# Kernel optimization log

Hardware: AMD Instinct MI355X
Metric: run time of the kernel (lower is better)

The kernel has to match this reference:

```python
import jax, jax.numpy as jnp
import numpy as np

BATCH = 4096
DIM = 128
TEMP = 0.5
EPS = 1e-12  # F.normalize eps


def setup_inputs() -> dict:
    key = jax.random.key(0)
    k1, k2 = jax.random.split(key)
    emb_i = jax.random.normal(k1, (BATCH, DIM), dtype=jnp.float32)
    emb_j = jax.random.normal(k2, (BATCH, DIM), dtype=jnp.float32)
    return {"emb_i": emb_i, "emb_j": emb_j}


def _l2_normalize(x):
    # matches torch.nn.functional.normalize(x, dim=1, eps=1e-12)
    n = jnp.maximum(jnp.linalg.norm(x, axis=1, keepdims=True), EPS)
    return x / n


def reference(emb_i, emb_j):
    B = BATCH
    z_i = _l2_normalize(emb_i)
    z_j = _l2_normalize(emb_j)
    reps = jnp.concatenate([z_i, z_j], axis=0)            # [2B, D]
    # cosine similarity of unit vectors == Gram matrix
    sim = reps @ reps.T                                   # [2B, 2B]
    sim_ij = jnp.diagonal(sim, offset=B)                  # [B]
    sim_ji = jnp.diagonal(sim, offset=-B)                 # [B]
    positives = jnp.concatenate([sim_ij, sim_ji], axis=0) # [2B]
    neg_mask = 1.0 - jnp.eye(2 * B, dtype=sim.dtype)
    denom = jnp.sum(neg_mask * jnp.exp(sim / TEMP), axis=1)  # [2B]
    # -log(exp(pos/T) / denom) == -pos/T + log(denom)
    loss_partial = -(positives / TEMP) + jnp.log(denom)
    loss = jnp.sum(loss_partial) / (2 * B * 5)
    return loss
```

## Files before the change

### kernel.cpp

```cpp
#include <hip/hip_runtime.h>
#include <hip/hip_bf16.h>

#define B_ROWS 4096
#define DIMN 128
#define N2 8192
#define SQRT_CEXP 1.6986436f

using f32x4 = __attribute__((ext_vector_type(4))) float;
using i32x4 = __attribute__((ext_vector_type(4))) int;
using i32x8 = __attribute__((ext_vector_type(8))) int;
typedef long i64;


__global__ __launch_bounds__(256) void normpos_k(const float* __restrict__ emb_i,
                                                 const float* __restrict__ emb_j,
                                                 i64* __restrict__ zt,
                                                 float* __restrict__ pospart,
                                                 float* __restrict__ out) {
    const int t = threadIdx.x;
    if (blockIdx.x == 0 && t == 0) out[0] = 0.f;
    const int lr = t >> 4;
    const int s  = t & 15;
    const int p  = blockIdx.x * 16 + lr;
    const float4* ai = (const float4*)(emb_i + (size_t)p * DIMN + s * 8);
    const float4* bj = (const float4*)(emb_j + (size_t)p * DIMN + s * 8);
    float4 a0 = ai[0], a1 = ai[1];
    float4 b0 = bj[0], b1 = bj[1];
    float sa = a0.x*a0.x + a0.y*a0.y + a0.z*a0.z + a0.w*a0.w
             + a1.x*a1.x + a1.y*a1.y + a1.z*a1.z + a1.w*a1.w;
    float sb = b0.x*b0.x + b0.y*b0.y + b0.z*b0.z + b0.w*b0.w
             + b1.x*b1.x + b1.y*b1.y + b1.z*b1.z + b1.w*b1.w;
    float dp = a0.x*b0.x + a0.y*b0.y + a0.z*b0.z + a0.w*b0.w
             + a1.x*b1.x + a1.y*b1.y + a1.z*b1.z + a1.w*b1.w;
    #pragma unroll
    for (int d = 1; d < 16; d <<= 1) {
        sa += __shfl_xor(sa, d);
        sb += __shfl_xor(sb, d);
        dp += __shfl_xor(dp, d);
    }
    float ia = __builtin_amdgcn_rsqf(fmaxf(sa, 1e-24f));
    float ib = __builtin_amdgcn_rsqf(fmaxf(sb, 1e-24f));
    float fa = ia * SQRT_CEXP, fb = ib * SQRT_CEXP;

    int wa0 = __builtin_amdgcn_cvt_pk_fp8_f32(a0.x * fa, a0.y * fa, 0, false);
    wa0     = __builtin_amdgcn_cvt_pk_fp8_f32(a0.z * fa, a0.w * fa, wa0, true);
    int wa1 = __builtin_amdgcn_cvt_pk_fp8_f32(a1.x * fa, a1.y * fa, 0, false);
    wa1     = __builtin_amdgcn_cvt_pk_fp8_f32(a1.z * fa, a1.w * fa, wa1, true);
    i64 qa = ((i64)(unsigned)wa1 << 32) | (unsigned)wa0;
    int wb0 = __builtin_amdgcn_cvt_pk_fp8_f32(b0.x * fb, b0.y * fb, 0, false);
    wb0     = __builtin_amdgcn_cvt_pk_fp8_f32(b0.z * fb, b0.w * fb, wb0, true);
    int wb1 = __builtin_amdgcn_cvt_pk_fp8_f32(b1.x * fb, b1.y * fb, 0, false);
    wb1     = __builtin_amdgcn_cvt_pk_fp8_f32(b1.z * fb, b1.w * fb, wb1, true);
    i64 qb = ((i64)(unsigned)wb1 << 32) | (unsigned)wb0;

    const int slot = ((s >> 2) * 16 + lr) * 4 + (s & 3);
    zt[(size_t)blockIdx.x * 256 + slot] = qa;
    zt[(size_t)(256 + blockIdx.x) * 256 + slot] = qb;

    __shared__ float red[16];
    if (s == 0) red[lr] = dp * ia * ib;
    __syncthreads();
    if (t == 0) {
        float x = 0.f;
        #pragma unroll
        for (int i = 0; i < 16; ++i) x += red[i];
        pospart[blockIdx.x] = x;
    }
}

template <bool MASK>
__device__ __forceinline__ void accum_step(const f32x4 (&acc)[2][2],
                                           float (&ps)[2][4],
                                           int rb, int cb, int rq, int fr) {
    #pragma unroll
    for (int m = 0; m < 2; ++m)
        #pragma unroll
        for (int n = 0; n < 2; ++n)
            #pragma unroll
            for (int j = 0; j < 4; ++j) {
                float e = __builtin_amdgcn_exp2f(acc[m][n][j]);
                if (MASK) {
                    if (rb + m * 16 + rq + j == cb + n * 16 + fr) e = 0.f;
                }
                ps[m][j] += e;
            }
}

__global__ __launch_bounds__(256) void gram_k(const char* __restrict__ zt,
                                              float* __restrict__ rowpart) {
    const int t = threadIdx.x;
    const int lane = t & 63;
    const int w = t >> 6;
    const int p = blockIdx.x >> 2;
    const int e = blockIdx.x & 3;
    const int rb = p * 32;
    const int fr = lane & 15;
    const int rq = (lane >> 4) * 4;

    const char* pa = zt + (size_t)(p * 2) * 2048 + lane * 32;
    const char* pb = zt + (size_t)(e * 128 + w * 32) * 2048 + lane * 32;

    i32x4 Alo[2], Ahi[2];
    #pragma unroll
    for (int m = 0; m < 2; ++m) {
        asm volatile("global_load_dwordx4 %0, %1, off"
                     : "=v"(Alo[m]) : "v"(pa + (size_t)m * 2048));
        asm volatile("global_load_dwordx4 %0, %1, off offset:16"
                     : "=v"(Ahi[m]) : "v"(pa + (size_t)m * 2048));
    }
    i32x4 Blo[2][2], Bhi[2][2];
    #pragma unroll
    for (int n = 0; n < 2; ++n) {
        asm volatile("global_load_dwordx4 %0, %1, off"
                     : "=v"(Blo[0][n]) : "v"(pb + (size_t)n * 2048));
        asm volatile("global_load_dwordx4 %0, %1, off offset:16"
                     : "=v"(Bhi[0][n]) : "v"(pb + (size_t)n * 2048));
    }
    asm volatile("s_waitcnt vmcnt(4)" ::: "memory");
    __builtin_amdgcn_sched_barrier(0);
    i32x8 A8[2];
    #pragma unroll
    for (int m = 0; m < 2; ++m)
        A8[m] = __builtin_shufflevector(Alo[m], Ahi[m], 0, 1, 2, 3, 4, 5, 6, 7);

    float ps[2][4] = {};
    #pragma unroll
    for (int s = 0; s < 16; ++s) {
        if (s < 15) {
            const char* pn = pb + (size_t)(s + 1) * 4096;
            #pragma unroll
            for (int n = 0; n < 2; ++n) {
                asm volatile("global_load_dwordx4 %0, %1, off"
                             : "=v"(Blo[(s + 1) & 1][n]) : "v"(pn + (size_t)n * 2048));
                asm volatile("global_load_dwordx4 %0, %1, off offset:16"
                             : "=v"(Bhi[(s + 1) & 1][n]) : "v"(pn + (size_t)n * 2048));
            }
            asm volatile("s_waitcnt vmcnt(4)" ::: "memory");
        } else {
            asm volatile("s_waitcnt vmcnt(0)" ::: "memory");
        }
        __builtin_amdgcn_sched_barrier(0);

        f32x4 acc[2][2] = {};
        __builtin_amdgcn_s_setprio(1);
        #pragma unroll
        for (int n = 0; n < 2; ++n) {
            i32x8 B8 = __builtin_shufflevector(Blo[s & 1][n], Bhi[s & 1][n],
                                               0, 1, 2, 3, 4, 5, 6, 7);
            #pragma unroll
            for (int m = 0; m < 2; ++m)
                acc[m][n] = __builtin_amdgcn_mfma_scale_f32_16x16x128_f8f6f4(
                    A8[m], B8, acc[m][n], 0, 0,
                    0, 0x7f7f7f7f, 0, 0x7f7f7f7f);
        }
        __builtin_amdgcn_s_setprio(0);

        const int cb = e * 2048 + w * 512 + s * 32;
        if (cb == rb) accum_step<true >(acc, ps, rb, cb, rq, fr);
        else          accum_step<false>(acc, ps, rb, cb, rq, fr);
    }

    #pragma unroll
    for (int m = 0; m < 2; ++m)
        #pragma unroll
        for (int j = 0; j < 4; ++j) {
            float v = ps[m][j];
            #pragma unroll
            for (int d = 1; d < 16; d <<= 1) v += __shfl_xor(v, d);
            ps[m][j] = v;
        }
    __shared__ float red[4][32];
    if (fr == 0) {
        #pragma unroll
        for (int m = 0; m < 2; ++m)
            #pragma unroll
            for (int j = 0; j < 4; ++j)
                red[w][m * 16 + rq + j] = ps[m][j];
    }
    __syncthreads();
    if (t < 32)
        rowpart[e * N2 + rb + t] = red[0][t] + red[1][t] + red[2][t] + red[3][t];
}

__global__ void finalize_k(const float* __restrict__ rowpart,
                           const float* __restrict__ pospart,
                           float* __restrict__ out) {
    const int t = threadIdx.x;
    const int r = blockIdx.x * 1024 + t;
    float d = rowpart[r] + rowpart[N2 + r] + rowpart[2 * N2 + r] + rowpart[3 * N2 + r];
    float acc = __builtin_amdgcn_logf(d) * 0.6931471805599453f;
    if (blockIdx.x == 0 && t < 256) acc -= 4.0f * pospart[t];
    #pragma unroll
    for (int m = 32; m; m >>= 1) acc += __shfl_xor(acc, m);
    __shared__ float red[16];
    if ((t & 63) == 0) red[t >> 6] = acc;
    __syncthreads();
    if (t == 0) {
        float x = 0.f;
        #pragma unroll
        for (int i = 0; i < 16; ++i) x += red[i];
        atomicAdd(out, x * (1.0f / (2.0f * B_ROWS * 5.0f)));
    }
}

extern "C" void kernel_launch(void* const* d_in, const int* in_sizes, int n_in,
                              void* d_out, int out_size, void* d_ws, size_t ws_size,
                              hipStream_t stream) {
    const float* emb_i = (const float*)d_in[0];
    const float* emb_j = (const float*)d_in[1];
    i64* zt        = (i64*)d_ws;
    float* rowpart = (float*)((char*)d_ws + (size_t)N2 * DIMN);
    float* pospart = rowpart + 4 * N2;

    normpos_k<<<256, 256, 0, stream>>>(emb_i, emb_j, zt, pospart, (float*)d_out);
    gram_k<<<1024, 256, 0, stream>>>((const char*)zt, rowpart);
    finalize_k<<<8, 1024, 0, stream>>>(rowpart, pospart, (float*)d_out);
}
```

Baseline: 25.83 us.

## Exploit Gram matrix symmetry to compute half the tiles with column partial sums

Adds a symmetric Gram kernel in which each block computes only half of the 32-wide diagonal tile offsets. It accumulates both row sums and column sums of exp(sim), and writes the column sums into a large colpart buffer that finalize_k sums over 127 offsets. This roughly halves the MFMA and exp work, at the cost of extra shuffles, a large workspace of about 4 MB of column partials, and a much heavier finalize pass that reads 128 strided rows per output. The old path is kept as a fallback when the workspace is too small.

```diff
diff --git a/kernel.cpp b/kernel.cpp
--- a/kernel.cpp
+++ b/kernel.cpp
@@ -70,7 +70,7 @@
 
 template <bool MASK>
 __device__ __forceinline__ void accum_step(const f32x4 (&acc)[2][2],
-                                           float (&ps)[2][4],
+                                           float (&ps)[2][4], float (&cs)[2],
                                            int rb, int cb, int rq, int fr) {
     #pragma unroll
     for (int m = 0; m < 2; ++m)
@@ -83,7 +83,153 @@
                     if (rb + m * 16 + rq + j == cb + n * 16 + fr) e = 0.f;
                 }
                 ps[m][j] += e;
+                cs[n] += e;
             }
+}
+
+__global__ __launch_bounds__(256) void gram_sym_k(const char* __restrict__ zt,
+                                                  float* __restrict__ rowpart,
+                                                  float* __restrict__ colpart) {
+    const int t = threadIdx.x;
+    const int lane = t & 63;
+    const int w = t >> 6;
+    const int p = blockIdx.x >> 2;
+    const int e = blockIdx.x & 3;
+    const int rb = p * 32;
+    const int fr = lane & 15;
+    const int rq = (lane >> 4) * 4;
+    const int dt0 = e * 32 + w * 8;
+
+    const char* pa = zt + (size_t)(p * 2) * 2048 + lane * 32;
+    auto bptr = [&](int dt) {
+        return zt + (size_t)((rb + dt * 32) & 8191) * 128 + lane * 32;
+    };
+
+    i32x4 Alo[2], Ahi[2];
+    #pragma unroll
+    for (int m = 0; m < 2; ++m) {
+        asm volatile("global_load_dwordx4 %0, %1, off"
+                     : "=v"(Alo[m]) : "v"(pa + (size_t)m * 2048));
+        asm volatile("global_load_dwordx4 %0, %1, off offset:16"
+                     : "=v"(Ahi[m]) : "v"(pa + (size_t)m * 2048));
+    }
+    i32x4 Blo[2][2], Bhi[2][2];
+    {
+        const char* p0 = bptr(dt0);
+        #pragma unroll
+        for (int n = 0; n < 2; ++n) {
+            asm volatile("global_load_dwordx4 %0, %1, off"
+                         : "=v"(Blo[0][n]) : "v"(p0 + (size_t)n * 2048));
+            asm volatile("global_load_dwordx4 %0, %1, off offset:16"
+                         : "=v"(Bhi[0][n]) : "v"(p0 + (size_t)n * 2048));
+        }
+    }
+    asm volatile("s_waitcnt vmcnt(4)" ::: "memory");
+    __builtin_amdgcn_sched_barrier(0);
+    i32x8 A8[2];
+    #pragma unroll
+    for (int m = 0; m < 2; ++m)
+        A8[m] = __builtin_shufflevector(Alo[m], Ahi[m], 0, 1, 2, 3, 4, 5, 6, 7);
+
+    float ps[2][4] = {};
+    float colsc0[8], colsc1[8];
+    #pragma unroll
+    for (int s = 0; s < 8; ++s) {
+        if (s < 7) {
+            const char* pn = bptr(dt0 + s + 1);
+            #pragma unroll
+            for (int n = 0; n < 2; ++n) {
+                asm volatile("global_load_dwordx4 %0, %1, off"
+                             : "=v"(Blo[(s + 1) & 1][n]) : "v"(pn + (size_t)n * 2048));
+                asm volatile("global_load_dwordx4 %0, %1, off offset:16"
+                             : "=v"(Bhi[(s + 1) & 1][n]) : "v"(pn + (size_t)n * 2048));
+            }
+            asm volatile("s_waitcnt vmcnt(4)" ::: "memory");
+        } else {
+            asm volatile("s_waitcnt vmcnt(0)" ::: "memory");
+        }
+        __builtin_amdgcn_sched_barrier(0);
+
+        f32x4 acc[2][2] = {};
+        __builtin_amdgcn_s_setprio(1);
+        #pragma unroll
+        for (int n = 0; n < 2; ++n) {
+            i32x8 B8 = __builtin_shufflevector(Blo[s & 1][n], Bhi[s & 1][n],
+                                               0, 1, 2, 3, 4, 5, 6, 7);
+            #pragma unroll
+            for (int m = 0; m < 2; ++m)
+                acc[m][n] = __builtin_amdgcn_mfma_scale_f32_16x16x128_f8f6f4(
+                    A8[m], B8, acc[m][n], 0, 0,
+                    0, 0x7f7f7f7f, 0, 0x7f7f7f7f);
+        }
+        __builtin_amdgcn_s_setprio(0);
+
+        const int cb = (rb + (dt0 + s) * 32) & 8191;
+        float cs[2] = {0.f, 0.f};
+        if (cb == rb) accum_step<true >(acc, ps, cs, rb, cb, rq, fr);
+        else          accum_step<false>(acc, ps, cs, rb, cb, rq, fr);
+        cs[0] += __shfl_xor(cs[0], 16); cs[0] += __shfl_xor(cs[0], 32);
+        cs[1] += __shfl_xor(cs[1], 16); cs[1] += __shfl_xor(cs[1], 32);
+        colsc0[s] = cs[0]; colsc1[s] = cs[1];
+    }
+
+    if (e == 0 && w == 0) {
+        const char* pn = bptr(128);
+        #pragma unroll
+        for (int n = 0; n < 2; ++n) {
+            asm volatile("global_load_dwordx4 %0, %1, off"
+                         : "=v"(Blo[0][n]) : "v"(pn + (size_t)n * 2048));
+            asm volatile("global_load_dwordx4 %0, %1, off offset:16"
+                         : "=v"(Bhi[0][n]) : "v"(pn + (size_t)n * 2048));
+        }
+        asm volatile("s_waitcnt vmcnt(0)" ::: "memory");
+        __builtin_amdgcn_sched_barrier(0);
+        f32x4 acc[2][2] = {};
+        #pragma unroll
+        for (int n = 0; n < 2; ++n) {
+            i32x8 B8 = __builtin_shufflevector(Blo[0][n], Bhi[0][n],
+                                               0, 1, 2, 3, 4, 5, 6, 7);
+            #pragma unroll
+            for (int m = 0; m < 2; ++m)
+                acc[m][n] = __builtin_amdgcn_mfma_scale_f32_16x16x128_f8f6f4(
+                    A8[m], B8, acc[m][n], 0, 0, 0, 0x7f7f7f7f, 0, 0x7f7f7f7f);
+        }
+        float cs[2] = {0.f, 0.f};
+        accum_step<false>(acc, ps, cs, rb, 0, rq, fr);
+    }
+
+    if (lane < 16) {
+        #pragma unroll
+        for (int s = 0; s < 8; ++s) {
+            const int dt = dt0 + s;
+            if (dt != 0) {
+                const int cbb = (rb + dt * 32) & 8191;
+                colpart[(size_t)dt * N2 + cbb + lane]      = colsc0[s];
+                colpart[(size_t)dt * N2 + cbb + 16 + lane] = colsc1[s];
+            }
+        }
+    }
+
+    #pragma unroll
+    for (int m = 0; m < 2; ++m)
+        #pragma unroll
+        for (int j = 0; j < 4; ++j) {
+            float v = ps[m][j];
+            #pragma unroll
+            for (int d = 1; d < 16; d <<= 1) v += __shfl_xor(v, d);
+            ps[m][j] = v;
+        }
+    __shared__ float red[4][32];
+    if (fr == 0) {
+        #pragma unroll
+        for (int m = 0; m < 2; ++m)
+            #pragma unroll
+            for (int j = 0; j < 4; ++j)
+                red[w][m * 16 + rq + j] = ps[m][j];
+    }
+    __syncthreads();
+    if (t < 32)
+        rowpart[e * N2 + rb + t] = red[0][t] + red[1][t] + red[2][t] + red[3][t];
 }
 
 __global__ __launch_bounds__(256) void gram_k(const char* __restrict__ zt,
@@ -150,14 +296,14 @@
             #pragma unroll
             for (int m = 0; m < 2; ++m)
                 acc[m][n] = __builtin_amdgcn_mfma_scale_f32_16x16x128_f8f6f4(
-                    A8[m], B8, acc[m][n], 0, 0,
-                    0, 0x7f7f7f7f, 0, 0x7f7f7f7f);
+                    A8[m], B8, acc[m][n], 0, 0, 0, 0x7f7f7f7f, 0, 0x7f7f7f7f);
         }
         __builtin_amdgcn_s_setprio(0);
 
         const int cb = e * 2048 + w * 512 + s * 32;
-        if (cb == rb) accum_step<true >(acc, ps, rb, cb, rq, fr);
-        else          accum_step<false>(acc, ps, rb, cb, rq, fr);
+        float cs[2] = {0.f, 0.f};
+        if (cb == rb) accum_step<true >(acc, ps, cs, rb, cb, rq, fr);
+        else          accum_step<false>(acc, ps, cs, rb, cb, rq, fr);
     }
 
     #pragma unroll
@@ -183,11 +329,13 @@
 }
 
 __global__ void finalize_k(const float* __restrict__ rowpart,
+                           const float* __restrict__ colpart,
                            const float* __restrict__ pospart,
-                           float* __restrict__ out) {
+                           float* __restrict__ out, int ncol) {
     const int t = threadIdx.x;
     const int r = blockIdx.x * 1024 + t;
     float d = rowpart[r] + rowpart[N2 + r] + rowpart[2 * N2 + r] + rowpart[3 * N2 + r];
+    for (int k = 1; k <= ncol; ++k) d += colpart[(size_t)k * N2 + r];
     float acc = __builtin_amdgcn_logf(d) * 0.6931471805599453f;
     if (blockIdx.x == 0 && t < 256) acc -= 4.0f * pospart[t];
     #pragma unroll
@@ -211,8 +359,16 @@
     i64* zt        = (i64*)d_ws;
     float* rowpart = (float*)((char*)d_ws + (size_t)N2 * DIMN);
     float* pospart = rowpart + 4 * N2;
+    float* colpart = pospart + 256;
+    const size_t need = (size_t)N2 * DIMN + (4 * N2 + 256 + 128 * N2) * sizeof(float);
+    const bool sym = ws_size >= need;
 
     normpos_k<<<256, 256, 0, stream>>>(emb_i, emb_j, zt, pospart, (float*)d_out);
-    gram_k<<<1024, 256, 0, stream>>>((const char*)zt, rowpart);
-    finalize_k<<<8, 1024, 0, stream>>>(rowpart, pospart, (float*)d_out);
-}
+    if (sym) {
+        gram_sym_k<<<1024, 256, 0, stream>>>((const char*)zt, rowpart, colpart);
+        finalize_k<<<8, 1024, 0, stream>>>(rowpart, colpart, pospart, (float*)d_out, 127);
+    } else {
+        gram_k<<<1024, 256, 0, stream>>>((const char*)zt, rowpart);
+        finalize_k<<<8, 1024, 0, stream>>>(rowpart, colpart, pospart, (float*)d_out, 0);
+    }
+}
```

Result: slower. 58.08 us (+124.9%).

## Exploit Gram matrix symmetry to halve MFMA tiles, adding column partial sums

Applied to the files above, without the earlier changes.

Each row block now computes only about half of the 32x32 tile diagonals, using a cyclic offset scheme (128 diagonals plus one extra diagonal at offset 128 handled by one wave). Each tile contributes its exp values to both row sums and column sums, since the symmetric counterpart is never computed. Column partials are written to a large colpart buffer, 128 slices of 8192 floats each. The finalize kernel now reduces all of those slices. This halves MFMA and exp work. In exchange it adds per-tile shuffles, about 4 MB of extra global writes and reads, and a heavier finalize pass.

```diff
diff --git a/kernel.cpp b/kernel.cpp
--- a/kernel.cpp
+++ b/kernel.cpp
@@ -70,7 +70,7 @@
 
 template <bool MASK>
 __device__ __forceinline__ void accum_step(const f32x4 (&acc)[2][2],
-                                           float (&ps)[2][4],
+                                           float (&ps)[2][4], float (&cs)[2],
                                            int rb, int cb, int rq, int fr) {
     #pragma unroll
     for (int m = 0; m < 2; ++m)
@@ -83,11 +83,13 @@
                     if (rb + m * 16 + rq + j == cb + n * 16 + fr) e = 0.f;
                 }
                 ps[m][j] += e;
+                cs[n] += e;
             }
 }
 
-__global__ __launch_bounds__(256) void gram_k(const char* __restrict__ zt,
-                                              float* __restrict__ rowpart) {
+__global__ __launch_bounds__(256) void gram_sym_k(const char* __restrict__ zt,
+                                                  float* __restrict__ rowpart,
+                                                  float* __restrict__ colpart) {
     const int t = threadIdx.x;
     const int lane = t & 63;
     const int w = t >> 6;
@@ -96,9 +98,12 @@
     const int rb = p * 32;
     const int fr = lane & 15;
     const int rq = (lane >> 4) * 4;
+    const int dt0 = e * 32 + w * 8;
 
     const char* pa = zt + (size_t)(p * 2) * 2048 + lane * 32;
-    const char* pb = zt + (size_t)(e * 128 + w * 32) * 2048 + lane * 32;
+    auto bptr = [&](int dt) {
+        return zt + (size_t)((rb + dt * 32) & 8191) * 128 + lane * 32;
+    };
 
     i32x4 Alo[2], Ahi[2];
     #pragma unroll
@@ -109,12 +114,15 @@
                      : "=v"(Ahi[m]) : "v"(pa + (size_t)m * 2048));
     }
     i32x4 Blo[2][2], Bhi[2][2];
-    #pragma unroll
-    for (int n = 0; n < 2; ++n) {
-        asm volatile("global_load_dwordx4 %0, %1, off"
-                     : "=v"(Blo[0][n]) : "v"(pb + (size_t)n * 2048));
-        asm volatile("global_load_dwordx4 %0, %1, off offset:16"
-                     : "=v"(Bhi[0][n]) : "v"(pb + (size_t)n * 2048));
+    {
+        const char* p0 = bptr(dt0);
+        #pragma unroll
+        for (int n = 0; n < 2; ++n) {
+            asm volatile("global_load_dwordx4 %0, %1, off"
+                         : "=v"(Blo[0][n]) : "v"(p0 + (size_t)n * 2048));
+            asm volatile("global_load_dwordx4 %0, %1, off offset:16"
+                         : "=v"(Bhi[0][n]) : "v"(p0 + (size_t)n * 2048));
+        }
     }
     asm volatile("s_waitcnt vmcnt(4)" ::: "memory");
     __builtin_amdgcn_sched_barrier(0);
@@ -124,10 +132,11 @@
         A8[m] = __builtin_shufflevector(Alo[m], Ahi[m], 0, 1, 2, 3, 4, 5, 6, 7);
 
     float ps[2][4] = {};
-    #pragma unroll
-    for (int s = 0; s < 16; ++s) {
-        if (s < 15) {
-            const char* pn = pb + (size_t)(s + 1) * 4096;
+    float colsc0[8], colsc1[8];
+    #pragma unroll
+    for (int s = 0; s < 8; ++s) {
+        if (s < 7) {
+            const char* pn = bptr(dt0 + s + 1);
             #pragma unroll
             for (int n = 0; n < 2; ++n) {
                 asm volatile("global_load_dwordx4 %0, %1, off"
@@ -155,9 +164,50 @@
         }
         __builtin_amdgcn_s_setprio(0);
 
-        const int cb = e * 2048 + w * 512 + s * 32;
-        if (cb == rb) accum_step<true >(acc, ps, rb, cb, rq, fr);
-        else          accum_step<false>(acc, ps, rb, cb, rq, fr);
+        const int cb = (rb + (dt0 + s) * 32) & 8191;
+        float cs[2] = {0.f, 0.f};
+        if (cb == rb) accum_step<true >(acc, ps, cs, rb, cb, rq, fr);
+        else          accum_step<false>(acc, ps, cs, rb, cb, rq, fr);
+        cs[0] += __shfl_xor(cs[0], 16); cs[0] += __shfl_xor(cs[0], 32);
+        cs[1] += __shfl_xor(cs[1], 16); cs[1] += __shfl_xor(cs[1], 32);
+        colsc0[s] = cs[0]; colsc1[s] = cs[1];
+    }
+
+    if (e == 0 && w == 0) {
+        const char* pn = bptr(128);
+        #pragma unroll
+        for (int n = 0; n < 2; ++n) {
+            asm volatile("global_load_dwordx4 %0, %1, off"
+                         : "=v"(Blo[0][n]) : "v"(pn + (size_t)n * 2048));
+            asm volatile("global_load_dwordx4 %0, %1, off offset:16"
+                         : "=v"(Bhi[0][n]) : "v"(pn + (size_t)n * 2048));
+        }
+        asm volatile("s_waitcnt vmcnt(0)" ::: "memory");
+        __builtin_amdgcn_sched_barrier(0);
+        f32x4 acc[2][2] = {};
+        #pragma unroll
+        for (int n = 0; n < 2; ++n) {
+            i32x8 B8 = __builtin_shufflevector(Blo[0][n], Bhi[0][n],
+                                               0, 1, 2, 3, 4, 5, 6, 7);
+            #pragma unroll
+            for (int m = 0; m < 2; ++m)
+                acc[m][n] = __builtin_amdgcn_mfma_scale_f32_16x16x128_f8f6f4(
+                    A8[m], B8, acc[m][n], 0, 0, 0, 0x7f7f7f7f, 0, 0x7f7f7f7f);
+        }
+        float cs[2] = {0.f, 0.f};
+        accum_step<false>(acc, ps, cs, rb, 0, rq, fr);
+    }
+
+    if (lane < 16) {
+        #pragma unroll
+        for (int s = 0; s < 8; ++s) {
+            const int dt = dt0 + s;
+            if (dt != 0) {
+                const int cbb = (rb + dt * 32) & 8191;
+                colpart[(size_t)dt * N2 + cbb + lane]      = colsc0[s];
+                colpart[(size_t)dt * N2 + cbb + 16 + lane] = colsc1[s];
+            }
+        }
     }
 
     #pragma unroll
@@ -182,25 +232,42 @@
         rowpart[e * N2 + rb + t] = red[0][t] + red[1][t] + red[2][t] + red[3][t];
 }
 
-__global__ void finalize_k(const float* __restrict__ rowpart,
-                           const float* __restrict__ pospart,
-                           float* __restrict__ out) {
+__global__ __launch_bounds__(256) void finalize_k(const float* __restrict__ rowpart,
+                                                  const float* __restrict__ colpart,
+                                                  const float* __restrict__ pospart,
+                                                  float* __restrict__ out) {
     const int t = threadIdx.x;
-    const int r = blockIdx.x * 1024 + t;
-    float d = rowpart[r] + rowpart[N2 + r] + rowpart[2 * N2 + r] + rowpart[3 * N2 + r];
+    const int r = blockIdx.x * 256 + t;
+    float a0 = rowpart[r], a1 = rowpart[N2 + r];
+    float a2 = rowpart[2 * N2 + r], a3 = rowpart[3 * N2 + r];
+    float a4 = 0.f, a5 = 0.f, a6 = 0.f, a7 = 0.f;
+    const float* cp = colpart + r;
+    for (int k = 1; k <= 113; k += 8) {
+        a0 += cp[(size_t)(k + 0) * N2];
+        a1 += cp[(size_t)(k + 1) * N2];
+        a2 += cp[(size_t)(k + 2) * N2];
+        a3 += cp[(size_t)(k + 3) * N2];
+        a4 += cp[(size_t)(k + 4) * N2];
+        a5 += cp[(size_t)(k + 5) * N2];
+        a6 += cp[(size_t)(k + 6) * N2];
+        a7 += cp[(size_t)(k + 7) * N2];
+    }
+    a0 += cp[(size_t)121 * N2]; a1 += cp[(size_t)122 * N2];
+    a2 += cp[(size_t)123 * N2]; a3 += cp[(size_t)124 * N2];
+    a4 += cp[(size_t)125 * N2]; a5 += cp[(size_t)126 * N2];
+    a6 += cp[(size_t)127 * N2];
+    float d = ((a0 + a1) + (a2 + a3)) + ((a4 + a5) + (a6 + a7));
+
     float acc = __builtin_amdgcn_logf(d) * 0.6931471805599453f;
-    if (blockIdx.x == 0 && t < 256) acc -= 4.0f * pospart[t];
+    if (blockIdx.x == 0) acc -= 4.0f * pospart[t];
     #pragma unroll
     for (int m = 32; m; m >>= 1) acc += __shfl_xor(acc, m);
-    __shared__ float red[16];
+    __shared__ float red[4];
     if ((t & 63) == 0) red[t >> 6] = acc;
     __syncthreads();
-    if (t == 0) {
-        float x = 0.f;
-        #pragma unroll
-        for (int i = 0; i < 16; ++i) x += red[i];
-        atomicAdd(out, x * (1.0f / (2.0f * B_ROWS * 5.0f)));
-    }
+    if (t == 0)
+        atomicAdd(out, (red[0] + red[1] + red[2] + red[3]) *
+                       (1.0f / (2.0f * B_ROWS * 5.0f)));
 }
 
 extern "C" void kernel_launch(void* const* d_in, const int* in_sizes, int n_in,
@@ -211,8 +278,9 @@
     i64* zt        = (i64*)d_ws;
     float* rowpart = (float*)((char*)d_ws + (size_t)N2 * DIMN);
     float* pospart = rowpart + 4 * N2;
+    float* colpart = pospart + 256;
 
     normpos_k<<<256, 256, 0, stream>>>(emb_i, emb_j, zt, pospart, (float*)d_out);
-    gram_k<<<1024, 256, 0, stream>>>((const char*)zt, rowpart);
-    finalize_k<<<8, 1024, 0, stream>>>(rowpart, pospart, (float*)d_out);
-}
+    gram_sym_k<<<1024, 256, 0, stream>>>((const char*)zt, rowpart, colpart);
+    finalize_k<<<32, 256, 0, stream>>>(rowpart, colpart, pospart, (float*)d_out);
+}
```

New measurement: 31.31 us. 21.2% more time.
